# Kernel optimization log

Hardware: AMD Instinct MI355X
Metric: run time of the kernel (lower is better)

Reference implementation:

```python
import jax, jax.numpy as jnp
import numpy as np

D_MODEL, D_STATE, D_CONV, EXPAND = 1024, 16, 4, 2
D_INNER = EXPAND * D_MODEL
DT_RANK = (D_MODEL + 15) // 16  # 64
B_SZ, SEQLEN = 2, 2048


def setup_inputs() -> dict:
    key = jax.random.key(0)
    ks = jax.random.split(key, 10)
    import math
    # dt bias init as in module
    dt = jnp.exp(jax.random.uniform(ks[8], (D_INNER,)) * (math.log(0.1) - math.log(0.001)) + math.log(0.001))
    dt = jnp.clip(dt, 1e-4, None)
    inv_dt = dt + jnp.log(-jnp.expm1(-dt))
    A_log = jnp.log(jnp.tile(jnp.arange(1, D_STATE + 1, dtype=jnp.float32)[None, :], (D_INNER, 1)))
    s = lambda k, shp, scale: jax.random.normal(k, shp, dtype=jnp.float32) * scale
    return {
        "hidden_states": jax.random.normal(ks[0], (B_SZ, SEQLEN, D_MODEL), dtype=jnp.float32),
        "in_proj_w": s(ks[1], (2 * D_INNER, D_MODEL), D_MODEL ** -0.5),
        "conv_w": s(ks[2], (D_INNER, D_CONV), D_CONV ** -0.5),
        "conv_b": s(ks[3], (D_INNER,), 0.02),
        "x_proj_w": s(ks[4], (DT_RANK + 2 * D_STATE, D_INNER), D_INNER ** -0.5),
        "dt_proj_w": jax.random.uniform(ks[5], (D_INNER, DT_RANK), minval=-DT_RANK ** -0.5, maxval=DT_RANK ** -0.5),
        "dt_proj_b": inv_dt,
        "A_log": A_log,
        "D": jnp.ones((D_INNER,), dtype=jnp.float32),
        "out_proj_w": s(ks[6], (D_MODEL, D_INNER), D_INNER ** -0.5),
    }


def _mamba_fwd(hidden_states, in_proj_w, conv_w, conv_b, x_proj_w,
               dt_proj_w, dt_proj_b, A_log, D, out_proj_w):
    B, L, _ = hidden_states.shape
    silu = jax.nn.silu
    # in projection: (B, 2*d_inner, L)
    xz = jnp.einsum('bld,ed->bel', hidden_states, in_proj_w)
    x, z = xz[:, :D_INNER, :], xz[:, D_INNER:, :]
    # depthwise causal conv1d, kernel size d_conv, left padding d_conv-1
    x_pad = jnp.pad(x, ((0, 0), (0, 0), (D_CONV - 1, 0)))
    xc = sum(conv_w[None, :, k, None] * x_pad[:, :, k:k + L] for k in range(D_CONV))
    x = silu(xc + conv_b[None, :, None])  # (B, d_inner, L)
    xt = jnp.swapaxes(x, 1, 2)            # (B, L, d_inner)
    # x_proj -> dt, B, C
    x_dbl = jnp.einsum('bld,ed->ble', xt, x_proj_w)
    dt_lo = x_dbl[..., :DT_RANK]
    Bm = x_dbl[..., DT_RANK:DT_RANK + D_STATE]   # (B, L, n)
    Cm = x_dbl[..., DT_RANK + D_STATE:]           # (B, L, n)
    delta = jax.nn.softplus(jnp.einsum('blr,dr->bld', dt_lo, dt_proj_w) + dt_proj_b)
    A = -jnp.exp(A_log.astype(jnp.float32))       # (d_inner, n)

    def step(h, inp):
        d_t, B_t, C_t, x_t = inp                  # (B,d) (B,n) (B,n) (B,d)
        dA = jnp.exp(d_t[..., None] * A)          # (B, d, n)
        h = dA * h + (d_t * x_t)[..., None] * B_t[:, None, :]
        y = jnp.einsum('bdn,bn->bd', h, C_t)
        return h, y

    h0 = jnp.zeros((B, D_INNER, D_STATE), dtype=jnp.float32)
    xs = (jnp.swapaxes(delta, 0, 1), jnp.swapaxes(Bm, 0, 1),
          jnp.swapaxes(Cm, 0, 1), jnp.swapaxes(xt, 0, 1))
    _, ys = jax.lax.scan(step, h0, xs)            # ys: (L, B, d_inner)
    y = jnp.swapaxes(ys, 0, 1) + D * xt           # skip connection D*x
    y = y * silu(jnp.swapaxes(z, 1, 2))           # gate
    return jnp.einsum('bld,md->blm', y, out_proj_w)


def reference(hidden_states, in_proj_w, conv_w, conv_b, x_proj_w,
              dt_proj_w, dt_proj_b, A_log, D, out_proj_w):
    return _mamba_fwd(hidden_states, in_proj_w, conv_w, conv_b, x_proj_w,
                      dt_proj_w, dt_proj_b, A_log, D, out_proj_w)
```

## Files before the change

kernel.cpp:

```cpp
#include <hip/hip_runtime.h>
#include <math.h>


#define DMODEL 1024
#define DINNER 2048
#define DSTATE 16
#define DTRANK 64
#define BSZ    2
#define LSEQ   2048
#define NCHUNK 64
#define CLEN   32
#define SPLITK 16
#define KCH    (DINNER / SPLITK)
#define XDBL_N 96
#define XDBL_SZ (BSZ*LSEQ*XDBL_N)
#define NROW16 (BSZ*DINNER*DSTATE)

typedef __attribute__((ext_vector_type(8))) short bf16x8;
typedef __attribute__((ext_vector_type(8))) unsigned short u16x8;
typedef __attribute__((ext_vector_type(4))) unsigned short u16x4;
typedef __attribute__((ext_vector_type(4))) float f32x4;

__device__ __forceinline__ float silu_f(float v) {
    return v / (1.f + __expf(-v));
}
__device__ __forceinline__ float softplus_f(float v) {
    return (v > 20.f) ? v : log1pf(expf(v));
}
__device__ __forceinline__ unsigned short f2bf(float f) {
    unsigned int u = __float_as_uint(f);
    unsigned int r = (u + 0x7fffu + ((u >> 16) & 1u)) >> 16;
    return (unsigned short)r;
}
__device__ __forceinline__ float bf2f(unsigned short u) {
    return __uint_as_float(((unsigned int)u) << 16);
}
__device__ __forceinline__ void gl_lds16(const void* g, void* l) {
    __builtin_amdgcn_global_load_lds(
        (const __attribute__((address_space(1))) unsigned int*)g,
        (__attribute__((address_space(3))) unsigned int*)l, 16, 0, 0);
}
__device__ __forceinline__ void cast8(const float* __restrict__ src,
                                      unsigned short* __restrict__ dst, size_t i) {
    float4 a = ((const float4*)src)[2 * i];
    float4 b = ((const float4*)src)[2 * i + 1];
    u16x8 v;
    v[0] = f2bf(a.x); v[1] = f2bf(a.y); v[2] = f2bf(a.z); v[3] = f2bf(a.w);
    v[4] = f2bf(b.x); v[5] = f2bf(b.y); v[6] = f2bf(b.z); v[7] = f2bf(b.w);
    *(u16x8*)(dst + 8 * i) = v;
}

__global__ __launch_bounds__(256) void cast_all(
    const float* __restrict__ hidden, const float* __restrict__ ipw,
    const float* __restrict__ opw, const float* __restrict__ dtw,
    const float* __restrict__ xpw,
    unsigned short* __restrict__ hbf, unsigned short* __restrict__ wbf,
    unsigned short* __restrict__ owbf, unsigned short* __restrict__ dtwbf,
    unsigned short* __restrict__ xpwbf)
{
    int bid = blockIdx.x;
    if (bid < 2048) {
        cast8(hidden, hbf, (size_t)bid * 256 + threadIdx.x);
    } else if (bid < 4096) {
        cast8(ipw, wbf, (size_t)(bid - 2048) * 256 + threadIdx.x);
    } else if (bid < 5120) {
        cast8(opw, owbf, (size_t)(bid - 4096) * 256 + threadIdx.x);
    } else if (bid < 5184) {
        cast8(dtw, dtwbf, (size_t)(bid - 5120) * 256 + threadIdx.x);
    } else {
        size_t i = (size_t)(bid - 5184) * 256 + threadIdx.x;
        size_t o = i * 8;
        int row = (int)(o >> 11);
        u16x8 v = {0, 0, 0, 0, 0, 0, 0, 0};
        if (row < 96) {
            float4 a = ((const float4*)xpw)[2 * i];
            float4 b = ((const float4*)xpw)[2 * i + 1];
            v[0] = f2bf(a.x); v[1] = f2bf(a.y); v[2] = f2bf(a.z); v[3] = f2bf(a.w);
            v[4] = f2bf(b.x); v[5] = f2bf(b.y); v[6] = f2bf(b.z); v[7] = f2bf(b.w);
        }
        *(u16x8*)(xpwbf + o) = v;
    }
}

template<int EPI>
__global__ __launch_bounds__(256) void gemm_bf16(
    const short* __restrict__ A, const short* __restrict__ B,
    float* __restrict__ C, int ldc,
    unsigned short* __restrict__ xb, unsigned short* __restrict__ zb,
    const float* __restrict__ bias, int K)
{
    __shared__ __align__(16) short As[128 * 32];
    __shared__ __align__(16) short Bs[128 * 32];
    const int t = threadIdx.x;
    const int wave = t >> 6, lane = t & 63;
    const int m0 = blockIdx.y * 128, n0 = blockIdx.x * 128;
    const int wm = (wave & 1) * 64, wn = (wave >> 1) * 64;
    const int srow = t >> 2;
    const int sq = (t & 3) * 16;

    const short* Ag = A + (size_t)(m0 + srow) * K;
    const short* Bg = B + (size_t)(n0 + srow) * K;
    char* AsL0 = (char*)As + wave * 1024;
    char* AsL1 = (char*)As + 4096 + wave * 1024;
    char* BsL0 = (char*)Bs + wave * 1024;
    char* BsL1 = (char*)Bs + 4096 + wave * 1024;

    const int quad = lane >> 4, l16 = lane & 15;
    const int aoff = (wm + l16) * 32 + quad * 8;
    const int boff = (wn + l16) * 32 + quad * 8;

    f32x4 acc[4][4];
#pragma unroll
    for (int i = 0; i < 4; i++)
#pragma unroll
        for (int j = 0; j < 4; j++) {
            f32x4 z = {0.f, 0.f, 0.f, 0.f};
            acc[i][j] = z;
        }

    for (int k0 = 0; k0 < K; k0 += 32) {
        __syncthreads();
        gl_lds16((const char*)(Ag + k0) + sq, AsL0);
        gl_lds16((const char*)(Ag + (size_t)64 * K + k0) + sq, AsL1);
        gl_lds16((const char*)(Bg + k0) + sq, BsL0);
        gl_lds16((const char*)(Bg + (size_t)64 * K + k0) + sq, BsL1);
        __syncthreads();
        bf16x8 af[4], bfr[4];
#pragma unroll
        for (int i = 0; i < 4; i++) {
            af[i]  = *(const bf16x8*)(As + aoff + i * 16 * 32);
            bfr[i] = *(const bf16x8*)(Bs + boff + i * 16 * 32);
        }
#pragma unroll
        for (int i = 0; i < 4; i++)
#pragma unroll
            for (int j = 0; j < 4; j++)
                acc[i][j] = __builtin_amdgcn_mfma_f32_16x16x32_bf16(
                    af[i], bfr[j], acc[i][j], 0, 0, 0);
    }

#pragma unroll
    for (int i = 0; i < 4; i++) {
        int mrow = m0 + wm + i * 16 + quad * 4;
#pragma unroll
        for (int j = 0; j < 4; j++) {
            int n = n0 + wn + j * 16 + l16;
            if (EPI == 1) {
                unsigned short* dst = (n0 < DINNER) ? xb : zb;
                int nn = (n0 < DINNER) ? n : (n - DINNER);
#pragma unroll
                for (int r = 0; r < 4; r++)
                    dst[(size_t)(mrow + r) * DINNER + nn] = f2bf(acc[i][j][r]);
            } else if (EPI == 2) {
                float bv = bias[n];
#pragma unroll
                for (int r = 0; r < 4; r++)
                    C[(size_t)(mrow + r) * ldc + n] =
                        softplus_f(acc[i][j][r] + bv);
            } else {
#pragma unroll
                for (int r = 0; r < 4; r++)
                    C[(size_t)(mrow + r) * ldc + n] = acc[i][j][r];
            }
        }
    }
}

__global__ __launch_bounds__(256) void gemm_n64(
    const short* __restrict__ A, const short* __restrict__ B,
    float* __restrict__ C, int ldc, int K)
{
    __shared__ __align__(16) short As[128 * 32];
    __shared__ __align__(16) short Bs[64 * 32];
    const int t = threadIdx.x;
    const int wave = t >> 6, lane = t & 63;
    const int m0 = blockIdx.y * 128, n0 = blockIdx.x * 64;
    const int wm = wave * 32;
    const int srow = t >> 2;
    const int sq = (t & 3) * 16;

    const short* Ag = A + (size_t)(m0 + srow) * K;
    const short* Bg = B + (size_t)(n0 + srow) * K;
    char* AsL0 = (char*)As + wave * 1024;
    char* AsL1 = (char*)As + 4096 + wave * 1024;
    char* BsL0 = (char*)Bs + wave * 1024;

    const int quad = lane >> 4, l16 = lane & 15;

    f32x4 acc[2][4];
#pragma unroll
    for (int i = 0; i < 2; i++)
#pragma unroll
        for (int j = 0; j < 4; j++) {
            f32x4 z = {0.f, 0.f, 0.f, 0.f};
            acc[i][j] = z;
        }

    for (int k0 = 0; k0 < K; k0 += 32) {
        __syncthreads();
        gl_lds16((const char*)(Ag + k0) + sq, AsL0);
        gl_lds16((const char*)(Ag + (size_t)64 * K + k0) + sq, AsL1);
        gl_lds16((const char*)(Bg + k0) + sq, BsL0);
        __syncthreads();
        bf16x8 af[2], bfr[4];
#pragma unroll
        for (int i = 0; i < 2; i++)
            af[i] = *(const bf16x8*)(As + (wm + i * 16 + l16) * 32 + quad * 8);
#pragma unroll
        for (int j = 0; j < 4; j++)
            bfr[j] = *(const bf16x8*)(Bs + (j * 16 + l16) * 32 + quad * 8);
#pragma unroll
        for (int i = 0; i < 2; i++)
#pragma unroll
            for (int j = 0; j < 4; j++)
                acc[i][j] = __builtin_amdgcn_mfma_f32_16x16x32_bf16(
                    af[i], bfr[j], acc[i][j], 0, 0, 0);
    }

#pragma unroll
    for (int i = 0; i < 2; i++) {
        int mrow = m0 + wm + i * 16 + quad * 4;
#pragma unroll
        for (int j = 0; j < 4; j++) {
            int n = n0 + j * 16 + l16;
#pragma unroll
            for (int r = 0; r < 4; r++)
                C[(size_t)(mrow + r) * ldc + n] = acc[i][j][r];
        }
    }
}

__global__ __launch_bounds__(256) void gemm_xproj(
    const short* __restrict__ Abf, const short* __restrict__ Bbf,
    float* __restrict__ ppart)
{
    __shared__ __align__(16) short As[128 * 32];
    __shared__ __align__(16) short Bs[128 * 32];
    const int t = threadIdx.x;
    const int wave = t >> 6, lane = t & 63;
    const int m0 = blockIdx.x * 128;
    const int kc = blockIdx.y;
    const int srow = t >> 2;
    const int sq = (t & 3) * 16;

    const short* Ag = Abf + (size_t)(m0 + srow) * DINNER;
    const short* Bg = Bbf + (size_t)srow * DINNER;
    char* AsL0 = (char*)As + wave * 1024;
    char* AsL1 = (char*)As + 4096 + wave * 1024;
    char* BsL0 = (char*)Bs + wave * 1024;
    char* BsL1 = (char*)Bs + 4096 + wave * 1024;

    const int quad = lane >> 4, l16 = lane & 15;
    const int wm = wave * 32;

    f32x4 acc[2][6];
#pragma unroll
    for (int i = 0; i < 2; i++)
#pragma unroll
        for (int j = 0; j < 6; j++) {
            f32x4 z = {0.f, 0.f, 0.f, 0.f};
            acc[i][j] = z;
        }

    for (int k0 = kc * KCH; k0 < kc * KCH + KCH; k0 += 32) {
        __syncthreads();
        gl_lds16((const char*)(Ag + k0) + sq, AsL0);
        gl_lds16((const char*)(Ag + (size_t)64 * DINNER + k0) + sq, AsL1);
        gl_lds16((const char*)(Bg + k0) + sq, BsL0);
        gl_lds16((const char*)(Bg + (size_t)64 * DINNER + k0) + sq, BsL1);
        __syncthreads();
        bf16x8 af[2], bfr[6];
#pragma unroll
        for (int i = 0; i < 2; i++)
            af[i] = *(const bf16x8*)(As + (wm + i * 16 + l16) * 32 + quad * 8);
#pragma unroll
        for (int j = 0; j < 6; j++)
            bfr[j] = *(const bf16x8*)(Bs + (j * 16 + l16) * 32 + quad * 8);
#pragma unroll
        for (int i = 0; i < 2; i++)
#pragma unroll
            for (int j = 0; j < 6; j++)
                acc[i][j] = __builtin_amdgcn_mfma_f32_16x16x32_bf16(
                    af[i], bfr[j], acc[i][j], 0, 0, 0);
    }

    float* dst = ppart + (size_t)kc * XDBL_SZ;
#pragma unroll
    for (int i = 0; i < 2; i++) {
        int mrow = m0 + wm + i * 16 + quad * 4;
#pragma unroll
        for (int j = 0; j < 6; j++) {
            int n = j * 16 + l16;
#pragma unroll
            for (int r = 0; r < 4; r++)
                dst[(size_t)(mrow + r) * XDBL_N + n] = acc[i][j][r];
        }
    }
}

__global__ __launch_bounds__(256) void reduce_xdbl(
    const float* __restrict__ ppart, float* __restrict__ xdbl,
    unsigned short* __restrict__ dtlobf)
{
    int i = blockIdx.x * 256 + threadIdx.x;
    float s = 0.f;
#pragma unroll
    for (int c = 0; c < SPLITK; c++) s += ppart[(size_t)c * XDBL_SZ + i];
    xdbl[i] = s;
    int m = i / XDBL_N;
    int n = i - m * XDBL_N;
    if (n < DTRANK) dtlobf[(size_t)m * DTRANK + n] = f2bf(s);
}

__global__ __launch_bounds__(256) void conv_silu(
    const unsigned short* __restrict__ xb, const float* __restrict__ convw,
    const float* __restrict__ convb, unsigned short* __restrict__ xtbf)
{
    int i = blockIdx.x * 256 + threadIdx.x;
    int c4 = i & 511;
    int m  = i >> 9;
    int l  = m & (LSEQ - 1);
    int ch = c4 * 4;
    const u16x4* base = (const u16x4*)xb + (size_t)m * 512 + c4;
    u16x4 vz = {0, 0, 0, 0};
    u16x4 v3 = base[0];
    u16x4 v2 = (l >= 1) ? base[-512]  : vz;
    u16x4 v1 = (l >= 2) ? base[-1024] : vz;
    u16x4 v0 = (l >= 3) ? base[-1536] : vz;
    float4 t0 = ((const float4*)convw)[ch + 0];
    float4 t1 = ((const float4*)convw)[ch + 1];
    float4 t2 = ((const float4*)convw)[ch + 2];
    float4 t3 = ((const float4*)convw)[ch + 3];
    float4 bv = ((const float4*)convb)[c4];
    u16x4 o;
    o[0] = f2bf(silu_f(bv.x + t0.x * bf2f(v0[0]) + t0.y * bf2f(v1[0]) +
                       t0.z * bf2f(v2[0]) + t0.w * bf2f(v3[0])));
    o[1] = f2bf(silu_f(bv.y + t1.x * bf2f(v0[1]) + t1.y * bf2f(v1[1]) +
                       t1.z * bf2f(v2[1]) + t1.w * bf2f(v3[1])));
    o[2] = f2bf(silu_f(bv.z + t2.x * bf2f(v0[2]) + t2.y * bf2f(v1[2]) +
                       t2.z * bf2f(v2[2]) + t2.w * bf2f(v3[2])));
    o[3] = f2bf(silu_f(bv.w + t3.x * bf2f(v0[3]) + t3.y * bf2f(v1[3]) +
                       t3.z * bf2f(v2[3]) + t3.w * bf2f(v3[3])));
    *(u16x4*)(xtbf + (size_t)m * DINNER + ch) = o;
}

__global__ __launch_bounds__(256) void scan_phaseA(
    const float* __restrict__ xdbl, const float* __restrict__ dlt,
    const unsigned short* __restrict__ xtbf, const float* __restrict__ A_log,
    float* __restrict__ Pbuf, float* __restrict__ Sbuf)
{
    __shared__ float Bsh[CLEN][16];
    const int d = blockIdx.x * 256 + threadIdx.x;
    const int c = blockIdx.y, b = blockIdx.z;
    if (threadIdx.x < CLEN * 4) {
        int lr = threadIdx.x >> 2, p = threadIdx.x & 3;
        const float* src = xdbl +
            ((size_t)b * LSEQ + (size_t)c * CLEN + lr) * XDBL_N + DTRANK + p * 4;
        *(float4*)&Bsh[lr][p * 4] = *(const float4*)src;
    }
    __syncthreads();

    float A[16], P[16], S[16];
#pragma unroll
    for (int q = 0; q < 4; q++) {
        float4 a4 = *(const float4*)(A_log + d * DSTATE + q * 4);
        A[4 * q] = -__expf(a4.x); A[4 * q + 1] = -__expf(a4.y);
        A[4 * q + 2] = -__expf(a4.z); A[4 * q + 3] = -__expf(a4.w);
    }
#pragma unroll
    for (int j = 0; j < 16; j++) { P[j] = 1.f; S[j] = 0.f; }

    size_t off = ((size_t)b * LSEQ + (size_t)c * CLEN) * DINNER + d;
    float dvn = dlt[off];
    float xvn = bf2f(xtbf[off]);
    for (int ll = 0; ll < CLEN; ++ll) {
        float dv = dvn, xv = xvn;
        if (ll + 1 < CLEN) {
            off += DINNER;
            dvn = dlt[off];
            xvn = bf2f(xtbf[off]);
        }
        float dx = dv * xv;
        f32x4 Bq[4];
#pragma unroll
        for (int q = 0; q < 4; q++) Bq[q] = *(const f32x4*)&Bsh[ll][q * 4];
#pragma unroll
        for (int j = 0; j < 16; j++) {
            float dA = __expf(dv * A[j]);
            P[j] *= dA;
            S[j] = fmaf(dA, S[j], dx * Bq[j >> 2][j & 3]);
        }
    }
    size_t o = ((size_t)c * BSZ * DINNER + (size_t)b * DINNER + d) * 16;
#pragma unroll
    for (int q = 0; q < 4; q++) {
        *(float4*)(Pbuf + o + q * 4) =
            make_float4(P[4 * q], P[4 * q + 1], P[4 * q + 2], P[4 * q + 3]);
        *(float4*)(Sbuf + o + q * 4) =
            make_float4(S[4 * q], S[4 * q + 1], S[4 * q + 2], S[4 * q + 3]);
    }
}

__global__ __launch_bounds__(256) void scan_phaseB(
    const float* __restrict__ Pbuf, const float* __restrict__ Sbuf,
    float* __restrict__ Hbuf)
{
    int r = blockIdx.x * 256 + threadIdx.x;
    float run = 0.f;
    for (int c = 0; c < NCHUNK; ++c) {
        size_t o = (size_t)c * NROW16 + r;
        Hbuf[o] = run;
        run = Pbuf[o] * run + Sbuf[o];
    }
}

__global__ __launch_bounds__(256) void scan_phaseC(
    const float* __restrict__ xdbl, const float* __restrict__ dlt,
    const unsigned short* __restrict__ xtbf, const unsigned short* __restrict__ zbf,
    const float* __restrict__ A_log, const float* __restrict__ Dvec,
    const float* __restrict__ Hbuf, unsigned short* __restrict__ ybf)
{
    __shared__ float BCsh[CLEN][32];
    const int d = blockIdx.x * 256 + threadIdx.x;
    const int c = blockIdx.y, b = blockIdx.z;
    {
        int lr = threadIdx.x >> 3, p = threadIdx.x & 7;
        const float* src = xdbl +
            ((size_t)b * LSEQ + (size_t)c * CLEN + lr) * XDBL_N + DTRANK;
        *(float4*)&BCsh[lr][p * 4] = *(const float4*)(src + p * 4);
    }
    __syncthreads();

    float A[16], h[16];
#pragma unroll
    for (int q = 0; q < 4; q++) {
        float4 a4 = *(const float4*)(A_log + d * DSTATE + q * 4);
        A[4 * q] = -__expf(a4.x); A[4 * q + 1] = -__expf(a4.y);
        A[4 * q + 2] = -__expf(a4.z); A[4 * q + 3] = -__expf(a4.w);
    }
    size_t o = ((size_t)c * BSZ * DINNER + (size_t)b * DINNER + d) * 16;
#pragma unroll
    for (int q = 0; q < 4; q++) {
        float4 h4 = *(const float4*)(Hbuf + o + q * 4);
        h[4 * q] = h4.x; h[4 * q + 1] = h4.y;
        h[4 * q + 2] = h4.z; h[4 * q + 3] = h4.w;
    }
    float Dd = Dvec[d];
    size_t off = ((size_t)b * LSEQ + (size_t)c * CLEN) * DINNER + d;
    float dvn = dlt[off];
    float xvn = bf2f(xtbf[off]);
    float zvn = bf2f(zbf[off]);
    size_t offc = off;
    for (int ll = 0; ll < CLEN; ++ll) {
        float dv = dvn, xv = xvn, zv = zvn;
        size_t offw = offc;
        if (ll + 1 < CLEN) {
            offc += DINNER;
            dvn = dlt[offc];
            xvn = bf2f(xtbf[offc]);
            zvn = bf2f(zbf[offc]);
        }
        float dx = dv * xv;
        f32x4 Bq[4], Cq[4];
#pragma unroll
        for (int q = 0; q < 4; q++) {
            Bq[q] = *(const f32x4*)&BCsh[ll][q * 4];
            Cq[q] = *(const f32x4*)&BCsh[ll][16 + q * 4];
        }
        float yp = 0.f;
#pragma unroll
        for (int j = 0; j < 16; j++) {
            float dA = __expf(dv * A[j]);
            h[j] = fmaf(dA, h[j], dx * Bq[j >> 2][j & 3]);
            yp = fmaf(h[j], Cq[j >> 2][j & 3], yp);
        }
        float yv = yp + Dd * xv;
        yv *= zv / (1.f + __expf(-zv));
        ybf[offw] = f2bf(yv);
    }
}

extern "C" void kernel_launch(void* const* d_in, const int* in_sizes, int n_in,
                              void* d_out, int out_size, void* d_ws, size_t ws_size,
                              hipStream_t stream)
{
    const float* hidden     = (const float*)d_in[0];
    const float* in_proj_w  = (const float*)d_in[1];
    const float* conv_w     = (const float*)d_in[2];
    const float* conv_b     = (const float*)d_in[3];
    const float* x_proj_w   = (const float*)d_in[4];
    const float* dt_proj_w  = (const float*)d_in[5];
    const float* dt_proj_b  = (const float*)d_in[6];
    const float* A_log      = (const float*)d_in[7];
    const float* Dvec       = (const float*)d_in[8];
    const float* out_proj_w = (const float*)d_in[9];
    float* out = (float*)d_out;

    const size_t MF = 1024 * 1024;
    float* ws = (float*)d_ws;
    unsigned short* xbf  = (unsigned short*)ws;
    float* dlt   = ws;
    unsigned short* zbf  = (unsigned short*)(ws + 8 * MF);
    unsigned short* xtbf = (unsigned short*)(ws + 12 * MF);
    float* Pbuf  = ws + 16 * MF;
    float* Sbuf  = ws + 20 * MF;
    float* Hbuf  = ws + 24 * MF;
    float* ppart = ws + 16 * MF;
    unsigned short* xpwbf  = (unsigned short*)(ws + 28 * MF);
    float* xdbl  = ws + 28 * MF + MF / 4;
    unsigned short* owbf   = (unsigned short*)(ws + 29 * MF);
    unsigned short* dtwbf  = (unsigned short*)(ws + 30 * MF);
    unsigned short* dtlobf = (unsigned short*)(ws + 30 * MF + MF / 4);
    unsigned short* hbf    = (unsigned short*)(ws + 31 * MF);
    unsigned short* wbf    = (unsigned short*)(ws + 33 * MF);
    unsigned short* ybf    = hbf;

    const int M = BSZ * LSEQ;

    cast_all<<<5312, 256, 0, stream>>>(hidden, in_proj_w, out_proj_w,
                                       dt_proj_w, x_proj_w,
                                       hbf, wbf, owbf, dtwbf, xpwbf);

    gemm_bf16<1><<<dim3(2 * DINNER / 128, M / 128), 256, 0, stream>>>(
        (const short*)hbf, (const short*)wbf, nullptr, 0, xbf, zbf,
        nullptr, DMODEL);

    conv_silu<<<(M * 512) / 256, 256, 0, stream>>>(xbf, conv_w, conv_b, xtbf);

    gemm_xproj<<<dim3(M / 128, SPLITK), 256, 0, stream>>>(
        (const short*)xtbf, (const short*)xpwbf, ppart);
    reduce_xdbl<<<XDBL_SZ / 256, 256, 0, stream>>>(ppart, xdbl, dtlobf);

    gemm_bf16<2><<<dim3(DINNER / 128, M / 128), 256, 0, stream>>>(
        (const short*)dtlobf, (const short*)dtwbf, dlt, DINNER,
        nullptr, nullptr, dt_proj_b, DTRANK);

    scan_phaseA<<<dim3(DINNER / 256, NCHUNK, BSZ), 256, 0, stream>>>(
        xdbl, dlt, xtbf, A_log, Pbuf, Sbuf);
    scan_phaseB<<<NROW16 / 256, 256, 0, stream>>>(Pbuf, Sbuf, Hbuf);
    scan_phaseC<<<dim3(DINNER / 256, NCHUNK, BSZ), 256, 0, stream>>>(
        xdbl, dlt, xtbf, zbf, A_log, Dvec, Hbuf, ybf);

    gemm_n64<<<dim3(DMODEL / 64, M / 128), 256, 0, stream>>>(
        (const short*)ybf, (const short*)owbf, out, DMODEL, DINNER);
}
```

Before: 343.6 us.

## Swizzle LDS tiles, transpose MFMA outputs for vector stores, store delta as bf16

XOR-swizzles the LDS layout in all three GEMM kernels to reduce bank conflicts on fragment reads. Swaps the MFMA operand order so each lane holds four consecutive output columns, which allows float4 or u16x4 vectorised stores instead of scalar strided stores. Stores the softplus delta as bf16 instead of fp32, halving its write and its reads in both scan phases at some cost in precision.

```diff
diff --git a/kernel.cpp b/kernel.cpp
--- a/kernel.cpp
+++ b/kernel.cpp
@@ -85,7 +85,6 @@
 template<int EPI>
 __global__ __launch_bounds__(256) void gemm_bf16(
     const short* __restrict__ A, const short* __restrict__ B,
-    float* __restrict__ C, int ldc,
     unsigned short* __restrict__ xb, unsigned short* __restrict__ zb,
     const float* __restrict__ bias, int K)
 {
@@ -96,7 +95,7 @@
     const int m0 = blockIdx.y * 128, n0 = blockIdx.x * 128;
     const int wm = (wave & 1) * 64, wn = (wave >> 1) * 64;
     const int srow = t >> 2;
-    const int sq = (t & 3) * 16;
+    const int sq = (((t & 3) ^ ((t >> 3) & 3)) * 16);
 
     const short* Ag = A + (size_t)(m0 + srow) * K;
     const short* Bg = B + (size_t)(n0 + srow) * K;
@@ -106,8 +105,10 @@
     char* BsL1 = (char*)Bs + 4096 + wave * 1024;
 
     const int quad = lane >> 4, l16 = lane & 15;
-    const int aoff = (wm + l16) * 32 + quad * 8;
-    const int boff = (wn + l16) * 32 + quad * 8;
+    const int swz = (l16 >> 1) & 3;
+    const int qs = (quad ^ swz) * 8;
+    const int aoff = (wm + l16) * 32 + qs;
+    const int boff = (wn + l16) * 32 + qs;
 
     f32x4 acc[4][4];
 #pragma unroll
@@ -136,31 +137,30 @@
 #pragma unroll
             for (int j = 0; j < 4; j++)
                 acc[i][j] = __builtin_amdgcn_mfma_f32_16x16x32_bf16(
-                    af[i], bfr[j], acc[i][j], 0, 0, 0);
+                    bfr[j], af[i], acc[i][j], 0, 0, 0);
     }
 
 #pragma unroll
     for (int i = 0; i < 4; i++) {
-        int mrow = m0 + wm + i * 16 + quad * 4;
+        int m = m0 + wm + i * 16 + l16;
 #pragma unroll
         for (int j = 0; j < 4; j++) {
-            int n = n0 + wn + j * 16 + l16;
+            int n = n0 + wn + j * 16 + quad * 4;
             if (EPI == 1) {
                 unsigned short* dst = (n0 < DINNER) ? xb : zb;
                 int nn = (n0 < DINNER) ? n : (n - DINNER);
-#pragma unroll
-                for (int r = 0; r < 4; r++)
-                    dst[(size_t)(mrow + r) * DINNER + nn] = f2bf(acc[i][j][r]);
-            } else if (EPI == 2) {
-                float bv = bias[n];
-#pragma unroll
-                for (int r = 0; r < 4; r++)
-                    C[(size_t)(mrow + r) * ldc + n] =
-                        softplus_f(acc[i][j][r] + bv);
+                u16x4 o;
+#pragma unroll
+                for (int r = 0; r < 4; r++) o[r] = f2bf(acc[i][j][r]);
+                *(u16x4*)(dst + (size_t)m * DINNER + nn) = o;
             } else {
-#pragma unroll
-                for (int r = 0; r < 4; r++)
-                    C[(size_t)(mrow + r) * ldc + n] = acc[i][j][r];
+                float4 bv = *(const float4*)(bias + n);
+                u16x4 o;
+                o[0] = f2bf(softplus_f(acc[i][j][0] + bv.x));
+                o[1] = f2bf(softplus_f(acc[i][j][1] + bv.y));
+                o[2] = f2bf(softplus_f(acc[i][j][2] + bv.z));
+                o[3] = f2bf(softplus_f(acc[i][j][3] + bv.w));
+                *(u16x4*)(xb + (size_t)m * DINNER + n) = o;
             }
         }
     }
@@ -177,7 +177,7 @@
     const int m0 = blockIdx.y * 128, n0 = blockIdx.x * 64;
     const int wm = wave * 32;
     const int srow = t >> 2;
-    const int sq = (t & 3) * 16;
+    const int sq = (((t & 3) ^ ((t >> 3) & 3)) * 16);
 
     const short* Ag = A + (size_t)(m0 + srow) * K;
     const short* Bg = B + (size_t)(n0 + srow) * K;
@@ -186,6 +186,8 @@
     char* BsL0 = (char*)Bs + wave * 1024;
 
     const int quad = lane >> 4, l16 = lane & 15;
+    const int swz = (l16 >> 1) & 3;
+    const int qs = (quad ^ swz) * 8;
 
     f32x4 acc[2][4];
 #pragma unroll
@@ -205,27 +207,27 @@
         bf16x8 af[2], bfr[4];
 #pragma unroll
         for (int i = 0; i < 2; i++)
-            af[i] = *(const bf16x8*)(As + (wm + i * 16 + l16) * 32 + quad * 8);
+            af[i] = *(const bf16x8*)(As + (wm + i * 16 + l16) * 32 + qs);
 #pragma unroll
         for (int j = 0; j < 4; j++)
-            bfr[j] = *(const bf16x8*)(Bs + (j * 16 + l16) * 32 + quad * 8);
+            bfr[j] = *(const bf16x8*)(Bs + (j * 16 + l16) * 32 + qs);
 #pragma unroll
         for (int i = 0; i < 2; i++)
 #pragma unroll
             for (int j = 0; j < 4; j++)
                 acc[i][j] = __builtin_amdgcn_mfma_f32_16x16x32_bf16(
-                    af[i], bfr[j], acc[i][j], 0, 0, 0);
+                    bfr[j], af[i], acc[i][j], 0, 0, 0);
     }
 
 #pragma unroll
     for (int i = 0; i < 2; i++) {
-        int mrow = m0 + wm + i * 16 + quad * 4;
+        int m = m0 + wm + i * 16 + l16;
 #pragma unroll
         for (int j = 0; j < 4; j++) {
-            int n = n0 + j * 16 + l16;
-#pragma unroll
-            for (int r = 0; r < 4; r++)
-                C[(size_t)(mrow + r) * ldc + n] = acc[i][j][r];
+            int n = n0 + j * 16 + quad * 4;
+            float4 v = make_float4(acc[i][j][0], acc[i][j][1],
+                                   acc[i][j][2], acc[i][j][3]);
+            *(float4*)(C + (size_t)m * ldc + n) = v;
         }
     }
 }
@@ -241,7 +243,7 @@
     const int m0 = blockIdx.x * 128;
     const int kc = blockIdx.y;
     const int srow = t >> 2;
-    const int sq = (t & 3) * 16;
+    const int sq = (((t & 3) ^ ((t >> 3) & 3)) * 16);
 
     const short* Ag = Abf + (size_t)(m0 + srow) * DINNER;
     const short* Bg = Bbf + (size_t)srow * DINNER;
@@ -251,6 +253,8 @@
     char* BsL1 = (char*)Bs + 4096 + wave * 1024;
 
     const int quad = lane >> 4, l16 = lane & 15;
+    const int swz = (l16 >> 1) & 3;
+    const int qs = (quad ^ swz) * 8;
     const int wm = wave * 32;
 
     f32x4 acc[2][6];
@@ -272,28 +276,28 @@
         bf16x8 af[2], bfr[6];
 #pragma unroll
         for (int i = 0; i < 2; i++)
-            af[i] = *(const bf16x8*)(As + (wm + i * 16 + l16) * 32 + quad * 8);
+            af[i] = *(const bf16x8*)(As + (wm + i * 16 + l16) * 32 + qs);
 #pragma unroll
         for (int j = 0; j < 6; j++)
-            bfr[j] = *(const bf16x8*)(Bs + (j * 16 + l16) * 32 + quad * 8);
+            bfr[j] = *(const bf16x8*)(Bs + (j * 16 + l16) * 32 + qs);
 #pragma unroll
         for (int i = 0; i < 2; i++)
 #pragma unroll
             for (int j = 0; j < 6; j++)
                 acc[i][j] = __builtin_amdgcn_mfma_f32_16x16x32_bf16(
-                    af[i], bfr[j], acc[i][j], 0, 0, 0);
+                    bfr[j], af[i], acc[i][j], 0, 0, 0);
     }
 
     float* dst = ppart + (size_t)kc * XDBL_SZ;
 #pragma unroll
     for (int i = 0; i < 2; i++) {
-        int mrow = m0 + wm + i * 16 + quad * 4;
+        int m = m0 + wm + i * 16 + l16;
 #pragma unroll
         for (int j = 0; j < 6; j++) {
-            int n = j * 16 + l16;
-#pragma unroll
-            for (int r = 0; r < 4; r++)
-                dst[(size_t)(mrow + r) * XDBL_N + n] = acc[i][j][r];
+            int n = j * 16 + quad * 4;
+            float4 v = make_float4(acc[i][j][0], acc[i][j][1],
+                                   acc[i][j][2], acc[i][j][3]);
+            *(float4*)(dst + (size_t)m * XDBL_N + n) = v;
         }
     }
 }
@@ -345,7 +349,7 @@
 }
 
 __global__ __launch_bounds__(256) void scan_phaseA(
-    const float* __restrict__ xdbl, const float* __restrict__ dlt,
+    const float* __restrict__ xdbl, const unsigned short* __restrict__ dltbf,
     const unsigned short* __restrict__ xtbf, const float* __restrict__ A_log,
     float* __restrict__ Pbuf, float* __restrict__ Sbuf)
 {
@@ -371,13 +375,13 @@
     for (int j = 0; j < 16; j++) { P[j] = 1.f; S[j] = 0.f; }
 
     size_t off = ((size_t)b * LSEQ + (size_t)c * CLEN) * DINNER + d;
-    float dvn = dlt[off];
+    float dvn = bf2f(dltbf[off]);
     float xvn = bf2f(xtbf[off]);
     for (int ll = 0; ll < CLEN; ++ll) {
         float dv = dvn, xv = xvn;
         if (ll + 1 < CLEN) {
             off += DINNER;
-            dvn = dlt[off];
+            dvn = bf2f(dltbf[off]);
             xvn = bf2f(xtbf[off]);
         }
         float dx = dv * xv;
@@ -415,7 +419,7 @@
 }
 
 __global__ __launch_bounds__(256) void scan_phaseC(
-    const float* __restrict__ xdbl, const float* __restrict__ dlt,
+    const float* __restrict__ xdbl, const unsigned short* __restrict__ dltbf,
     const unsigned short* __restrict__ xtbf, const unsigned short* __restrict__ zbf,
     const float* __restrict__ A_log, const float* __restrict__ Dvec,
     const float* __restrict__ Hbuf, unsigned short* __restrict__ ybf)
@@ -447,7 +451,7 @@
     }
     float Dd = Dvec[d];
     size_t off = ((size_t)b * LSEQ + (size_t)c * CLEN) * DINNER + d;
-    float dvn = dlt[off];
+    float dvn = bf2f(dltbf[off]);
     float xvn = bf2f(xtbf[off]);
     float zvn = bf2f(zbf[off]);
     size_t offc = off;
@@ -456,7 +460,7 @@
         size_t offw = offc;
         if (ll + 1 < CLEN) {
             offc += DINNER;
-            dvn = dlt[offc];
+            dvn = bf2f(dltbf[offc]);
             xvn = bf2f(xtbf[offc]);
             zvn = bf2f(zbf[offc]);
         }
@@ -498,8 +502,8 @@
 
     const size_t MF = 1024 * 1024;
     float* ws = (float*)d_ws;
-    unsigned short* xbf  = (unsigned short*)ws;
-    float* dlt   = ws;
+    unsigned short* xbf   = (unsigned short*)ws;
+    unsigned short* dltbf = (unsigned short*)ws;
     unsigned short* zbf  = (unsigned short*)(ws + 8 * MF);
     unsigned short* xtbf = (unsigned short*)(ws + 12 * MF);
     float* Pbuf  = ws + 16 * MF;
@@ -522,8 +526,7 @@
                                        hbf, wbf, owbf, dtwbf, xpwbf);
 
     gemm_bf16<1><<<dim3(2 * DINNER / 128, M / 128), 256, 0, stream>>>(
-        (const short*)hbf, (const short*)wbf, nullptr, 0, xbf, zbf,
-        nullptr, DMODEL);
+        (const short*)hbf, (const short*)wbf, xbf, zbf, nullptr, DMODEL);
 
     conv_silu<<<(M * 512) / 256, 256, 0, stream>>>(xbf, conv_w, conv_b, xtbf);
 
@@ -532,14 +535,14 @@
     reduce_xdbl<<<XDBL_SZ / 256, 256, 0, stream>>>(ppart, xdbl, dtlobf);
 
     gemm_bf16<2><<<dim3(DINNER / 128, M / 128), 256, 0, stream>>>(
-        (const short*)dtlobf, (const short*)dtwbf, dlt, DINNER,
-        nullptr, nullptr, dt_proj_b, DTRANK);
+        (const short*)dtlobf, (const short*)dtwbf, dltbf, nullptr,
+        dt_proj_b, DTRANK);
 
     scan_phaseA<<<dim3(DINNER / 256, NCHUNK, BSZ), 256, 0, stream>>>(
-        xdbl, dlt, xtbf, A_log, Pbuf, Sbuf);
+        xdbl, dltbf, xtbf, A_log, Pbuf, Sbuf);
     scan_phaseB<<<NROW16 / 256, 256, 0, stream>>>(Pbuf, Sbuf, Hbuf);
     scan_phaseC<<<dim3(DINNER / 256, NCHUNK, BSZ), 256, 0, stream>>>(
-        xdbl, dlt, xtbf, zbf, A_log, Dvec, Hbuf, ybf);
+        xdbl, dltbf, xtbf, zbf, A_log, Dvec, Hbuf, ybf);
 
     gemm_n64<<<dim3(DMODEL / 64, M / 128), 256, 0, stream>>>(
         (const short*)ybf, (const short*)owbf, out, DMODEL, DINNER);
```

Result: no change. 346.8 us (+0.9%).
